# Performance work log

Measured on AMD Instinct MI355X. Metric: run time of the kernel, lower is better.

The kernel has to match this reference:

```python
import jax, jax.numpy as jnp
import numpy as np

N = 50000; C = 128; H0 = 256; H1 = 128; EM = 1000000; ES = 200000
INTENSITY = 10.0


def _ln(x, g, b):
    mu = jnp.mean(x, -1, keepdims=True)
    var = jnp.mean((x - mu) ** 2, -1, keepdims=True)
    return (x - mu) / jnp.sqrt(var + 1e-5) * g + b


def _sp_w(w):
    # PositiveLinear: softplus(raw_weight) + epsilon
    return jax.nn.softplus(w) + 1e-6


def _monotone(x, w0, b0, w1, b1, w2, b2):
    # MonotoneMap dims [1,32,32,1], Softplus activations between layers
    h = jax.nn.softplus(x @ _sp_w(w0).T + b0)
    h = jax.nn.softplus(h @ _sp_w(w1).T + b1)
    return h @ _sp_w(w2).T + b2


def _forward(nodes_latent, nbrs_latent, message_edgestr,
             W0, b0, g0, be0, W1, b1, g1, be1,
             Wp, bp, Ww, bw, sim_scale, sim_shift, coeff_raw,
             mm_w0, mm_b0, mm_w1, mm_b1, mm_w2, mm_b2,
             sup_src, sup_dst, msg_src, msg_dst):
    Nn = nodes_latent.shape[0]
    Es = sup_src.shape[0]
    M = 2 * Es
    # ---- congruence_score ----
    sup_query = jnp.concatenate([sup_src, sup_dst])      # [M]
    sup_partner = jnp.concatenate([sup_dst, sup_src])    # [M]
    partner_index = jnp.full((Nn,), -1, jnp.int32).at[sup_partner].max(jnp.arange(M, dtype=jnp.int32))
    pidx = partner_index[msg_dst]
    valid = pidx >= 0                                    # isin(msg_dst, sup_partner)
    # per masked message edge, query node = sup_query[partner_index[msg_dst]]; invalid -> dump segment Nn
    q = jnp.where(valid, sup_query[jnp.clip(pidx, 0)], Nn)
    qg = jnp.where(valid, q, 0)                          # safe gather index
    unit = nodes_latent / jnp.maximum(jnp.linalg.norm(nodes_latent, axis=-1, keepdims=True), 1e-8)
    cos = jnp.sum(unit[qg] * unit[msg_src], -1)          # cosine_similarity, [EM]
    scores = INTENSITY * cos
    segmax = jax.ops.segment_max(scores, q, num_segments=Nn + 1)
    e = jnp.exp(scores - jax.lax.stop_gradient(segmax)[q])
    denom = jax.ops.segment_sum(e, q, num_segments=Nn + 1)
    weights = e / denom[q]                               # scatter_softmax over query node
    cnt = jnp.maximum(jax.ops.segment_sum(jnp.ones_like(cos), q, num_segments=Nn + 1)[:Nn], 1.0)
    cong_node = jax.ops.segment_sum(weights * cos, q, num_segments=Nn + 1)[:Nn] / cnt  # scatter_mean
    exist = cong_node[sup_src] + cong_node[sup_dst]      # [Es]
    mm = _monotone(cos[:, None], mm_w0, mm_b0, mm_w1, mm_b1, mm_w2, mm_b2)[:, 0]
    weighted_edges = mm * message_edgestr
    strength_node = jax.ops.segment_sum(weighted_edges, q, num_segments=Nn + 1)[:Nn] / cnt
    strength = strength_node[sup_src] + strength_node[sup_dst]  # computed, discarded by original forward
    del strength
    # ---- main forward ----
    a = nodes_latent[sup_src] + nodes_latent[sup_dst]
    m = nodes_latent[sup_src] * nodes_latent[sup_dst]
    combined = jnp.concatenate([a, m], -1)               # [Es, 2C]
    h = jax.nn.relu(_ln(combined @ W0 + b0, g0, be0))
    ef = jax.nn.relu(_ln(h @ W1 + b1, g1, be1))          # edge_features [Es, H1]
    nbrs_sim = jnp.sum(nbrs_latent[sup_src] * nbrs_latent[sup_dst], -1, keepdims=True)
    P_cong = sim_scale * (exist[:, None] + sim_shift)
    P_nbr = sim_scale * (nbrs_sim + sim_shift)
    P_dec = ef @ Wp + bp
    u_c = jax.nn.softplus(coeff_raw)
    coeff = u_c / u_c.sum()                              # SoftplusSimplex
    logits = coeff * jnp.concatenate([P_dec, P_nbr, P_cong], -1)
    strengths = jax.nn.relu(jnp.concatenate([ef, nbrs_sim], -1) @ Ww + bw)
    return logits, strengths, coeff


def setup_inputs() -> dict:
    key = jax.random.key(0)
    ks = jax.random.split(key, 16)
    d = {}
    d['nodes_latent'] = jax.random.normal(ks[0], (N, C), jnp.float32)
    d['nbrs_latent'] = jax.random.normal(ks[1], (N, C), jnp.float32)
    d['sup_src'] = jax.random.randint(ks[2], (ES,), 0, N)
    d['sup_dst'] = jax.random.randint(ks[3], (ES,), 0, N)
    d['msg_src'] = jax.random.randint(ks[4], (EM,), 0, N)
    d['msg_dst'] = jax.random.randint(ks[5], (EM,), 0, N)
    d['message_edgestr'] = jax.random.uniform(ks[6], (EM,), jnp.float32)
    def lin(k, fi, fo):
        s = 1.0 / np.sqrt(fi)
        k1, k2 = jax.random.split(k)
        return (jax.random.uniform(k1, (fi, fo), jnp.float32, -s, s),
                jax.random.uniform(k2, (fo,), jnp.float32, -s, s))
    d['W0'], d['b0'] = lin(ks[7], 2 * C, H0)
    d['g0'] = jnp.ones((H0,), jnp.float32); d['be0'] = jnp.zeros((H0,), jnp.float32)
    d['W1'], d['b1'] = lin(ks[8], H0, H1)
    d['g1'] = jnp.ones((H1,), jnp.float32); d['be1'] = jnp.zeros((H1,), jnp.float32)
    d['Wp'], d['bp'] = lin(ks[9], H1, 1)
    d['Ww'], d['bw'] = lin(ks[10], H1 + 1, 1)
    d['sim_scale'] = jnp.float32(1.0)
    d['sim_shift'] = jnp.float32(0.0)
    d['coeff_raw'] = jnp.full((3,), 1.0 / 3.0, jnp.float32)
    d['mm_w0'] = jax.random.normal(ks[11], (32, 1), jnp.float32) * 0.01
    d['mm_b0'] = jnp.zeros((32,), jnp.float32)
    d['mm_w1'] = jax.random.normal(ks[12], (32, 32), jnp.float32) * 0.01
    d['mm_b1'] = jnp.zeros((32,), jnp.float32)
    d['mm_w2'] = jax.random.normal(ks[13], (1, 32), jnp.float32) * 0.01
    d['mm_b2'] = jnp.zeros((1,), jnp.float32)
    return d


def reference(nodes_latent, nbrs_latent, sup_src, sup_dst, msg_src, msg_dst, message_edgestr,
              W0, b0, g0, be0, W1, b1, g1, be1, Wp, bp, Ww, bw,
              sim_scale, sim_shift, coeff_raw,
              mm_w0, mm_b0, mm_w1, mm_b1, mm_w2, mm_b2):
    return _forward(nodes_latent, nbrs_latent, message_edgestr,
                    W0, b0, g0, be0, W1, b1, g1, be1,
                    Wp, bp, Ww, bw, sim_scale, sim_shift, coeff_raw,
                    mm_w0, mm_b0, mm_w1, mm_b1, mm_w2, mm_b2,
                    sup_src, sup_dst, msg_src, msg_dst)
```

## Files before the change

### kernel.cpp

```cpp
#include <hip/hip_runtime.h>
#include <math.h>

namespace {

constexpr int NN  = 50000;
constexpr int CC  = 128;
constexpr int EMn = 1000000;
constexpr int ESn = 200000;
constexpr int MLPB = 256;
constexpr int WPB  = 12;
constexpr int NTILES = ESn / 16;
constexpr int NWAVES = MLPB * WPB;

using i32x4 = __attribute__((ext_vector_type(4))) int;

__device__ __forceinline__ float softplusf(float x) {
  return (x > 20.f) ? x : log1pf(expf(x));
}
__device__ __forceinline__ int sdot4i(unsigned a, unsigned b, int c) {
#if __has_builtin(__builtin_amdgcn_sdot4)
  return __builtin_amdgcn_sdot4((int)a, (int)b, c, false);
#else
  int r = c;
#pragma unroll
  for (int k = 0; k < 4; k++) {
    int xa = ((int)(a << (24 - 8 * k))) >> 24;
    int xb = ((int)(b << (24 - 8 * k))) >> 24;
    r += xa * xb;
  }
  return r;
#endif
}
__device__ __forceinline__ unsigned pack4(float a, float b, float c, float d) {
  int ia = __float2int_rn(a), ib = __float2int_rn(b);
  int ic = __float2int_rn(c), id = __float2int_rn(d);
  return (unsigned)(ia & 255) | ((unsigned)(ib & 255) << 8) |
         ((unsigned)(ic & 255) << 16) | ((unsigned)(id & 255) << 24);
}

__global__ void k_init(int* __restrict__ pidx, double* __restrict__ dencnt,
                       float* __restrict__ num) {
  int i = blockIdx.x * blockDim.x + threadIdx.x;
  if (i < NN) { pidx[i] = -1; dencnt[i] = 0.0; num[i] = 0.f; }
}

__global__ void k_cvtq(const float* __restrict__ nodes, const float* __restrict__ nbrs,
                       char* __restrict__ qnodes, char* __restrict__ qunit,
                       char* __restrict__ qnbrs, float* __restrict__ nscale,
                       float* __restrict__ nbscale) {
  int row = blockIdx.x * 16 + (threadIdx.x >> 4);
  int li = threadIdx.x & 15;
  if (row >= 2 * NN) return;
  bool isn = row < NN;
  int r = isn ? row : row - NN;
  const float* src = (isn ? nodes : nbrs) + (size_t)r * CC;
  float4 x0 = *(const float4*)(src + li * 8);
  float4 x1 = *(const float4*)(src + li * 8 + 4);
  float v[8] = {x0.x, x0.y, x0.z, x0.w, x1.x, x1.y, x1.z, x1.w};
  float amax = 0.f, sq = 0.f;
#pragma unroll
  for (int j = 0; j < 8; j++) { amax = fmaxf(amax, fabsf(v[j])); sq += v[j] * v[j]; }
#pragma unroll
  for (int off = 1; off < 16; off <<= 1) {
    amax = fmaxf(amax, __shfl_xor(amax, off, 64));
    sq += __shfl_xor(sq, off, 64);
  }
  amax = fmaxf(amax, 1e-8f);
  float rs = 127.f / amax;
  uint2 p;
  p.x = pack4(v[0] * rs, v[1] * rs, v[2] * rs, v[3] * rs);
  p.y = pack4(v[4] * rs, v[5] * rs, v[6] * rs, v[7] * rs);
  if (isn) {
    *(uint2*)(qnodes + (size_t)r * CC + li * 8) = p;
    float ru = 127.f / fmaxf(sqrtf(sq), 1e-8f);
    uint2 pu;
    pu.x = pack4(v[0] * ru, v[1] * ru, v[2] * ru, v[3] * ru);
    pu.y = pack4(v[4] * ru, v[5] * ru, v[6] * ru, v[7] * ru);
    *(uint2*)(qunit + (size_t)r * CC + li * 8) = pu;
    if (li == 0) nscale[r] = amax / 127.f;
  } else {
    *(uint2*)(qnbrs + (size_t)r * CC + li * 8) = p;
    if (li == 0) nbscale[r] = amax / 127.f;
  }
}

__global__ void k_partner(const int* __restrict__ ss, const int* __restrict__ sd,
                          int* __restrict__ pidx) {
  int i = blockIdx.x * blockDim.x + threadIdx.x;
  if (i >= 2 * ESn) return;
  int partner = (i < ESn) ? sd[i] : ss[i - ESn];
  atomicMax(&pidx[partner], i);
}

__global__ void k_qnode(const int* __restrict__ pidx, const int* __restrict__ ss,
                        const int* __restrict__ sd, int* __restrict__ qnode) {
  int n = blockIdx.x * blockDim.x + threadIdx.x;
  if (n >= NN) return;
  int pi = pidx[n];
  qnode[n] = (pi < 0) ? -1 : ((pi < ESn) ? ss[pi] : sd[pi - ESn]);
}

__global__ __launch_bounds__(256) void k_prep2(const float* __restrict__ W0,
                                               const float* __restrict__ W1,
                                               char* __restrict__ w0q, char* __restrict__ w1q,
                                               float* __restrict__ cs0, float* __restrict__ cs1) {
  __shared__ float wmax[4];
  int c = blockIdx.x;
  int k = threadIdx.x;
  bool is0 = c < 256;
  int col = is0 ? c : c - 256;
  float v = is0 ? W0[(size_t)k * 256 + col] : W1[(size_t)k * 128 + col];
  float am = fabsf(v);
#pragma unroll
  for (int off = 1; off < 64; off <<= 1) am = fmaxf(am, __shfl_xor(am, off, 64));
  if ((k & 63) == 0) wmax[k >> 6] = am;
  __syncthreads();
  float amax = fmaxf(fmaxf(wmax[0], wmax[1]), fmaxf(wmax[2], wmax[3]));
  amax = fmaxf(amax, 1e-12f);
  int q = __float2int_rn(v * (127.f / amax));
  char* dst = is0 ? w0q : w1q;
  dst[(size_t)col * 256 + ((((k >> 4) ^ (col & 15))) << 4) + (k & 15)] = (char)q;
  if (k == 0) (is0 ? cs0 : cs1)[col] = amax / 127.f;
}

__global__ void k_cong(const double* __restrict__ dencnt, const float* __restrict__ num,
                       float* __restrict__ cong) {
  int n = blockIdx.x * blockDim.x + threadIdx.x;
  if (n >= NN) return;
  double dc = dencnt[n];
  double cnt = floor(dc * (1.0 / 4294967296.0) + 0.5);
  double den = dc - cnt * 4294967296.0;
  cong[n] = (cnt > 0.0) ? (float)(((double)num[n] / fmax(den, 1e-30)) / cnt) : 0.f;
}

__global__ void k_finish(const int* __restrict__ ssrc, const int* __restrict__ sdst,
                         const float* __restrict__ cong, const float* __restrict__ sscale,
                         const float* __restrict__ sshift, const float* __restrict__ craw,
                         float* __restrict__ out) {
  int i = blockIdx.x * blockDim.x + threadIdx.x;
  float u0 = softplusf(craw[0]), u1 = softplusf(craw[1]), u2 = softplusf(craw[2]);
  float usum = u0 + u1 + u2;
  float c2 = u2 / usum;
  if (i < ESn)
    out[3 * i + 2] = c2 * (sscale[0] * (cong[ssrc[i]] + cong[sdst[i]] + sshift[0]));
  if (i == 0) {
    out[4 * ESn + 0] = u0 / usum;
    out[4 * ESn + 1] = u1 / usum;
    out[4 * ESn + 2] = c2;
  }
}

__global__ __launch_bounds__(768, 3) void k_big(
    const char* __restrict__ qnodes, const float* __restrict__ nscale,
    const char* __restrict__ qnbrs, const float* __restrict__ nbscale,
    const char* __restrict__ qunit, const int* __restrict__ qnode,
    const int* __restrict__ ssrc, const int* __restrict__ sdst,
    const int* __restrict__ ms, const int* __restrict__ md,
    double* __restrict__ dencnt, float* __restrict__ num,
    const char* __restrict__ w0q, const char* __restrict__ w1q,
    const float* __restrict__ cs0g, const float* __restrict__ cs1g,
    const float* __restrict__ b0, const float* __restrict__ g0, const float* __restrict__ be0,
    const float* __restrict__ b1, const float* __restrict__ g1, const float* __restrict__ be1,
    const float* __restrict__ Wp, const float* __restrict__ bp,
    const float* __restrict__ Ww, const float* __restrict__ bw,
    const float* __restrict__ sscale, const float* __restrict__ sshift,
    const float* __restrict__ craw, float* __restrict__ out) {
  __shared__ char  w0s[65536];
  __shared__ char  w1s[32768];
  __shared__ float prm[1792];
  __shared__ char  hln[WPB][4096];

  const int t = threadIdx.x;
  for (int i = t; i < 4096; i += 768) ((uint4*)w0s)[i] = ((const uint4*)w0q)[i];
  for (int i = t; i < 2048; i += 768) ((uint4*)w1s)[i] = ((const uint4*)w1q)[i];
  if (t < 256) { prm[t] = cs0g[t]; prm[256 + t] = b0[t]; prm[512 + t] = g0[t]; prm[768 + t] = be0[t]; }
  if (t < 128) { prm[1024 + t] = cs1g[t]; prm[1152 + t] = b1[t]; prm[1280 + t] = g1[t];
                 prm[1408 + t] = be1[t];  prm[1536 + t] = Wp[t]; prm[1664 + t] = Ww[t]; }
  __syncthreads();

  const int wv = t >> 6, l = t & 63;
  const int e16 = l & 15, ch = l >> 4;
  const int gw = blockIdx.x * WPB + wv;
  char* hw = hln[wv];

  float u0 = softplusf(craw[0]), u1 = softplusf(craw[1]), u2 = softplusf(craw[2]);
  float us = u0 + u1 + u2, c0 = u0 / us, c1 = u1 / us;
  float sc = sscale[0], sh = sshift[0], bp0 = bp[0], bw0 = bw[0], ww128 = Ww[128];

  for (int tile = gw; tile < NTILES; tile += NWAVES) {
    const int s0 = tile * 16;
    int eg = s0 + e16;
    int es = ssrc[eg], ed = sdst[eg];
    float sxs = nscale[es], sxd = nscale[ed];
    const uint4* xp = (const uint4*)(qnodes + (size_t)es * CC);
    const uint4* yp = (const uint4*)(qnodes + (size_t)ed * CC);
    uint4 X0 = xp[ch], X1 = xp[4 + ch], Y0 = yp[ch], Y1 = yp[4 + ch];
    const uint4* nxp = (const uint4*)(qnbrs + (size_t)es * CC);
    const uint4* nyp = (const uint4*)(qnbrs + (size_t)ed * CC);
    uint4 NX0 = nxp[2 * ch], NX1 = nxp[2 * ch + 1];
    uint4 NY0 = nyp[2 * ch], NY1 = nyp[2 * ch + 1];
    float nbs = nbscale[es] * nbscale[ed];

    int sa = 0;
    sa = sdot4i(NX0.x, NY0.x, sa); sa = sdot4i(NX0.y, NY0.y, sa);
    sa = sdot4i(NX0.z, NY0.z, sa); sa = sdot4i(NX0.w, NY0.w, sa);
    sa = sdot4i(NX1.x, NY1.x, sa); sa = sdot4i(NX1.y, NY1.y, sa);
    sa = sdot4i(NX1.z, NY1.z, sa); sa = sdot4i(NX1.w, NY1.w, sa);
    sa += __shfl_xor(sa, 16, 64); sa += __shfl_xor(sa, 32, 64);
    float nsim = (float)sa * nbs;

    unsigned xw[8] = {X0.x, X0.y, X0.z, X0.w, X1.x, X1.y, X1.z, X1.w};
    unsigned yw[8] = {Y0.x, Y0.y, Y0.z, Y0.w, Y1.x, Y1.y, Y1.z, Y1.w};

    float amax = 1e-8f;
#pragma unroll
    for (int d = 0; d < 8; d++)
#pragma unroll
      for (int b = 0; b < 4; b++) {
        float fx = (float)((int)(xw[d] << (24 - 8 * b)) >> 24) * sxs;
        float fy = (float)((int)(yw[d] << (24 - 8 * b)) >> 24) * sxd;
        amax = fmaxf(amax, fmaxf(fabsf(fx + fy), fabsf(fx * fy)));
      }
    amax = fmaxf(amax, __shfl_xor(amax, 16, 64));
    amax = fmaxf(amax, __shfl_xor(amax, 32, 64));
    float rqz = 127.f / amax, rsc = amax / 127.f;

    i32x4 fr[4];
#pragma unroll
    for (int half = 0; half < 2; half++) {
#pragma unroll
      for (int d = 0; d < 4; d++) {
        unsigned xd = xw[half * 4 + d], yd = yw[half * 4 + d];
        float a_[4], m_[4];
#pragma unroll
        for (int b = 0; b < 4; b++) {
          float fx = (float)((int)(xd << (24 - 8 * b)) >> 24) * sxs;
          float fy = (float)((int)(yd << (24 - 8 * b)) >> 24) * sxd;
          a_[b] = fx + fy; m_[b] = fx * fy;
        }
        fr[half][d]     = (int)pack4(a_[0] * rqz, a_[1] * rqz, a_[2] * rqz, a_[3] * rqz);
        fr[2 + half][d] = (int)pack4(m_[0] * rqz, m_[1] * rqz, m_[2] * rqz, m_[3] * rqz);
      }
    }
    float rsrow[4];
#pragma unroll
    for (int j = 0; j < 4; j++) rsrow[j] = __shfl(rsc, (ch << 2) + j, 64);

    i32x4 acc[16];
#pragma unroll
    for (int nf = 0; nf < 16; nf++) acc[nf] = (i32x4){0, 0, 0, 0};
#pragma unroll
    for (int s = 0; s < 4; s++) {
      int gofs = (((s * 4 + ch) ^ e16) << 4);
#pragma unroll
      for (int nf = 0; nf < 16; nf++) {
        i32x4 bfr = *(const i32x4*)&w0s[(nf * 16 + e16) * 256 + gofs];
        acc[nf] = __builtin_amdgcn_mfma_i32_16x16x64_i8(fr[s], bfr, acc[nf], 0, 0, 0);
      }
    }

    float sj[4] = {0, 0, 0, 0}, qj[4] = {0, 0, 0, 0};
#pragma unroll
    for (int nf = 0; nf < 16; nf++) {
      float cs = prm[nf * 16 + e16], bb = prm[256 + nf * 16 + e16];
#pragma unroll
      for (int j = 0; j < 4; j++) {
        float h = (float)acc[nf][j] * rsrow[j] * cs + bb;
        sj[j] += h; qj[j] += h * h;
      }
    }
    float mu[4], rstd[4];
#pragma unroll
    for (int j = 0; j < 4; j++) {
      float s = sj[j], q = qj[j];
#pragma unroll
      for (int off = 1; off < 16; off <<= 1) { s += __shfl_xor(s, off, 64); q += __shfl_xor(q, off, 64); }
      mu[j] = s * (1.f / 256.f);
      rstd[j] = rsqrtf(q * (1.f / 256.f) - mu[j] * mu[j] + 1e-5f);
    }
    float hmax[4] = {1e-8f, 1e-8f, 1e-8f, 1e-8f};
#pragma unroll
    for (int nf = 0; nf < 16; nf++) {
      float cs = prm[nf * 16 + e16], bb = prm[256 + nf * 16 + e16];
      float gg = prm[512 + nf * 16 + e16], be = prm[768 + nf * 16 + e16];
#pragma unroll
      for (int j = 0; j < 4; j++) {
        float h = (float)acc[nf][j] * rsrow[j] * cs + bb;
        float v = fmaxf((h - mu[j]) * rstd[j] * gg + be, 0.f);
        hmax[j] = fmaxf(hmax[j], v);
        acc[nf][j] = __float_as_int(v);
      }
    }
    float rq2[4], rs2[4];
#pragma unroll
    for (int j = 0; j < 4; j++) {
      float m = hmax[j];
#pragma unroll
      for (int off = 1; off < 16; off <<= 1) m = fmaxf(m, __shfl_xor(m, off, 64));
      rq2[j] = 127.f / m; rs2[j] = m / 127.f;
    }
#pragma unroll
    for (int nf = 0; nf < 16; nf++) {
#pragma unroll
      for (int j = 0; j < 4; j++) {
        int r = (ch << 2) + j;
        int qv = __float2int_rn(__int_as_float(acc[nf][j]) * rq2[j]);
        hw[r * 256 + ((nf ^ r) << 4) + e16] = (char)qv;
      }
    }

    i32x4 acc2[8];
#pragma unroll
    for (int nf = 0; nf < 8; nf++) acc2[nf] = (i32x4){0, 0, 0, 0};
#pragma unroll
    for (int s = 0; s < 4; s++) {
      int gofs = (((s * 4 + ch) ^ e16) << 4);
      i32x4 af = *(const i32x4*)&hw[e16 * 256 + gofs];
#pragma unroll
      for (int nf = 0; nf < 8; nf++) {
        i32x4 bfr = *(const i32x4*)&w1s[(nf * 16 + e16) * 256 + gofs];
        acc2[nf] = __builtin_amdgcn_mfma_i32_16x16x64_i8(af, bfr, acc2[nf], 0, 0, 0);
      }
    }

    float s2[4] = {0, 0, 0, 0}, q2[4] = {0, 0, 0, 0};
#pragma unroll
    for (int nf = 0; nf < 8; nf++) {
      float cs = prm[1024 + nf * 16 + e16], bb = prm[1152 + nf * 16 + e16];
#pragma unroll
      for (int j = 0; j < 4; j++) {
        float ef = (float)acc2[nf][j] * rs2[j] * cs + bb;
        s2[j] += ef; q2[j] += ef * ef;
      }
    }
    float mu2[4], rstd2[4];
#pragma unroll
    for (int j = 0; j < 4; j++) {
      float s = s2[j], q = q2[j];
#pragma unroll
      for (int off = 1; off < 16; off <<= 1) { s += __shfl_xor(s, off, 64); q += __shfl_xor(q, off, 64); }
      mu2[j] = s * (1.f / 128.f);
      rstd2[j] = rsqrtf(q * (1.f / 128.f) - mu2[j] * mu2[j] + 1e-5f);
    }
    float pd[4] = {0, 0, 0, 0}, ws_[4] = {0, 0, 0, 0};
#pragma unroll
    for (int nf = 0; nf < 8; nf++) {
      float cs = prm[1024 + nf * 16 + e16], bb = prm[1152 + nf * 16 + e16];
      float gg = prm[1280 + nf * 16 + e16], be = prm[1408 + nf * 16 + e16];
      float wp_ = prm[1536 + nf * 16 + e16], ww_ = prm[1664 + nf * 16 + e16];
#pragma unroll
      for (int j = 0; j < 4; j++) {
        float ef = (float)acc2[nf][j] * rs2[j] * cs + bb;
        float v = fmaxf((ef - mu2[j]) * rstd2[j] * gg + be, 0.f);
        pd[j] += v * wp_; ws_[j] += v * ww_;
      }
    }
#pragma unroll
    for (int j = 0; j < 4; j++)
#pragma unroll
      for (int off = 1; off < 16; off <<= 1) {
        pd[j] += __shfl_xor(pd[j], off, 64);
        ws_[j] += __shfl_xor(ws_[j], off, 64);
      }
    float nsr[4];
#pragma unroll
    for (int j = 0; j < 4; j++) nsr[j] = __shfl(nsim, (ch << 2) + j, 64);
    if (e16 == 0) {
#pragma unroll
      for (int j = 0; j < 4; j++) {
        int sidx = s0 + (ch << 2) + j;
        out[3 * sidx + 0] = c0 * (pd[j] + bp0);
        out[3 * sidx + 1] = c1 * (sc * (nsr[j] + sh));
        out[3 * ESn + sidx] = fmaxf(ws_[j] + nsr[j] * ww128 + bw0, 0.f);
      }
    }
  }

  const int li8 = l & 7, grp = l >> 3;
  for (int i = gw; i < EMn / 8; i += NWAVES) {
    int e = i * 8 + grp;
    int q = qnode[md[e]];
    if (q < 0) continue;
    int s = ms[e];
    uint4 a = ((const uint4*)(qunit + (size_t)q * CC))[li8];
    uint4 b = ((const uint4*)(qunit + (size_t)s * CC))[li8];
    int acc = 0;
    acc = sdot4i(a.x, b.x, acc); acc = sdot4i(a.y, b.y, acc);
    acc = sdot4i(a.z, b.z, acc); acc = sdot4i(a.w, b.w, acc);
    acc += __shfl_xor(acc, 1, 64);
    acc += __shfl_xor(acc, 2, 64);
    acc += __shfl_xor(acc, 4, 64);
    if (li8 == 0) {
      float cv = (float)acc * (1.0f / (127.f * 127.f));
      float wvv = expf(10.0f * cv);
      atomicAdd(&dencnt[q], (double)wvv + 4294967296.0);
      atomicAdd(&num[q], wvv * cv);
    }
  }
}

}

extern "C" void kernel_launch(void* const* d_in, const int* in_sizes, int n_in,
                              void* d_out, int out_size, void* d_ws, size_t ws_size,
                              hipStream_t stream) {
  (void)in_sizes; (void)n_in; (void)out_size; (void)ws_size;
  const float* nodes  = (const float*)d_in[0];
  const float* nbrs   = (const float*)d_in[1];
  const int* sup_src  = (const int*)d_in[2];
  const int* sup_dst  = (const int*)d_in[3];
  const int* msg_src  = (const int*)d_in[4];
  const int* msg_dst  = (const int*)d_in[5];
  const float* W0  = (const float*)d_in[7];
  const float* b0  = (const float*)d_in[8];
  const float* g0  = (const float*)d_in[9];
  const float* be0 = (const float*)d_in[10];
  const float* W1  = (const float*)d_in[11];
  const float* b1  = (const float*)d_in[12];
  const float* g1  = (const float*)d_in[13];
  const float* be1 = (const float*)d_in[14];
  const float* Wp  = (const float*)d_in[15];
  const float* bp  = (const float*)d_in[16];
  const float* Ww  = (const float*)d_in[17];
  const float* bw  = (const float*)d_in[18];
  const float* sscale = (const float*)d_in[19];
  const float* sshift = (const float*)d_in[20];
  const float* craw   = (const float*)d_in[21];
  float* out = (float*)d_out;

  char* p = (char*)d_ws;
  auto take = [&](size_t bytes) -> char* {
    char* r = p; p += (bytes + 255) & ~(size_t)255; return r;
  };
  char*   w0q     = take((size_t)256 * 256);
  char*   w1q     = take((size_t)128 * 256);
  float*  cs0     = (float*)take((size_t)256 * 4);
  float*  cs1     = (float*)take((size_t)128 * 4);
  char*   qnodes  = take((size_t)NN * CC);
  char*   qunit   = take((size_t)NN * CC);
  char*   qnbrs   = take((size_t)NN * CC);
  float*  nscale  = (float*)take((size_t)NN * 4);
  float*  nbscale = (float*)take((size_t)NN * 4);
  int*    pidx    = (int*)take((size_t)NN * 4);
  int*    qnode   = (int*)take((size_t)NN * 4);
  double* dencnt  = (double*)take((size_t)NN * 8);
  float*  num     = (float*)take((size_t)NN * 4);
  float*  cong    = (float*)take((size_t)NN * 4);

  k_init<<<(NN + 255) / 256, 256, 0, stream>>>(pidx, dencnt, num);
  k_cvtq<<<(2 * NN + 15) / 16, 256, 0, stream>>>(nodes, nbrs, qnodes, qunit, qnbrs,
                                                 nscale, nbscale);
  k_prep2<<<384, 256, 0, stream>>>(W0, W1, w0q, w1q, cs0, cs1);
  k_partner<<<(2 * ESn + 255) / 256, 256, 0, stream>>>(sup_src, sup_dst, pidx);
  k_qnode<<<(NN + 255) / 256, 256, 0, stream>>>(pidx, sup_src, sup_dst, qnode);
  k_big<<<MLPB, 768, 0, stream>>>(qnodes, nscale, qnbrs, nbscale, qunit, qnode,
                                  sup_src, sup_dst, msg_src, msg_dst, dencnt, num,
                                  w0q, w1q, cs0, cs1, b0, g0, be0, b1, g1, be1,
                                  Wp, bp, Ww, bw, sscale, sshift, craw, out);
  k_cong<<<(NN + 255) / 256, 256, 0, stream>>>(dencnt, num, cong);
  k_finish<<<(ESn + 255) / 256, 256, 0, stream>>>(sup_src, sup_dst, cong,
                                                  sscale, sshift, craw, out);
}
```

Before: 244.9 us.

## Prefetch next MLP tile gathers and restructure message-edge cosine loop

The support-edge MLP loop now issues the gathers for the next tile before computing the current one, so global-load latency overlaps the int8 matrix work. A separate pass precomputes each message edge's query node, with invalid edges sent to a zeroed dump row and dump accumulator slot. This removes the data-dependent skip and double indirection from the cosine loop, which now uses 4 lanes per edge with 16 edges per wave and exp2f. Launch bounds are relaxed to one block per SM to leave registers for the prefetch. The cost is an extra kernel, a 4 MB index array, and atomic work spent on invalid edges that land in the dump slot.

```diff
diff --git a/kernel.cpp b/kernel.cpp
--- a/kernel.cpp
+++ b/kernel.cpp
@@ -39,9 +39,11 @@
 }
 
 __global__ void k_init(int* __restrict__ pidx, double* __restrict__ dencnt,
-                       float* __restrict__ num) {
+                       float* __restrict__ num, char* __restrict__ qunit) {
   int i = blockIdx.x * blockDim.x + threadIdx.x;
-  if (i < NN) { pidx[i] = -1; dencnt[i] = 0.0; num[i] = 0.f; }
+  if (i < NN) pidx[i] = -1;
+  if (i <= NN) { dencnt[i] = 0.0; num[i] = 0.f; }
+  if (i < CC / 4) ((unsigned*)(qunit + (size_t)NN * CC))[i] = 0u;
 }
 
 __global__ void k_cvtq(const float* __restrict__ nodes, const float* __restrict__ nbrs,
@@ -100,6 +102,14 @@
   qnode[n] = (pi < 0) ? -1 : ((pi < ESn) ? ss[pi] : sd[pi - ESn]);
 }
 
+__global__ void k_qedge(const int* __restrict__ md, const int* __restrict__ qnode,
+                        int* __restrict__ qedge) {
+  int e = blockIdx.x * blockDim.x + threadIdx.x;
+  if (e >= EMn) return;
+  int q = qnode[md[e]];
+  qedge[e] = (q < 0) ? NN : q;
+}
+
 __global__ __launch_bounds__(256) void k_prep2(const float* __restrict__ W0,
                                                const float* __restrict__ W1,
                                                char* __restrict__ w0q, char* __restrict__ w1q,
@@ -150,12 +160,12 @@
   }
 }
 
-__global__ __launch_bounds__(768, 3) void k_big(
+__global__ __launch_bounds__(768, 1) void k_big(
     const char* __restrict__ qnodes, const float* __restrict__ nscale,
     const char* __restrict__ qnbrs, const float* __restrict__ nbscale,
-    const char* __restrict__ qunit, const int* __restrict__ qnode,
+    const char* __restrict__ qunit, const int* __restrict__ qedge,
     const int* __restrict__ ssrc, const int* __restrict__ sdst,
-    const int* __restrict__ ms, const int* __restrict__ md,
+    const int* __restrict__ ms,
     double* __restrict__ dencnt, float* __restrict__ num,
     const char* __restrict__ w0q, const char* __restrict__ w1q,
     const float* __restrict__ cs0g, const float* __restrict__ cs1g,
@@ -187,19 +197,24 @@
   float us = u0 + u1 + u2, c0 = u0 / us, c1 = u1 / us;
   float sc = sscale[0], sh = sshift[0], bp0 = bp[0], bw0 = bw[0], ww128 = Ww[128];
 
-  for (int tile = gw; tile < NTILES; tile += NWAVES) {
-    const int s0 = tile * 16;
-    int eg = s0 + e16;
+  int tile = gw;
+  float sxs = 0.f, sxd = 0.f, nbs = 0.f;
+  uint4 X0 = {}, X1 = {}, Y0 = {}, Y1 = {}, NX0 = {}, NX1 = {}, NY0 = {}, NY1 = {};
+  if (tile < NTILES) {
+    int eg = tile * 16 + e16;
     int es = ssrc[eg], ed = sdst[eg];
-    float sxs = nscale[es], sxd = nscale[ed];
+    sxs = nscale[es]; sxd = nscale[ed];
+    nbs = nbscale[es] * nbscale[ed];
     const uint4* xp = (const uint4*)(qnodes + (size_t)es * CC);
     const uint4* yp = (const uint4*)(qnodes + (size_t)ed * CC);
-    uint4 X0 = xp[ch], X1 = xp[4 + ch], Y0 = yp[ch], Y1 = yp[4 + ch];
+    X0 = xp[ch]; X1 = xp[4 + ch]; Y0 = yp[ch]; Y1 = yp[4 + ch];
     const uint4* nxp = (const uint4*)(qnbrs + (size_t)es * CC);
     const uint4* nyp = (const uint4*)(qnbrs + (size_t)ed * CC);
-    uint4 NX0 = nxp[2 * ch], NX1 = nxp[2 * ch + 1];
-    uint4 NY0 = nyp[2 * ch], NY1 = nyp[2 * ch + 1];
-    float nbs = nbscale[es] * nbscale[ed];
+    NX0 = nxp[2 * ch]; NX1 = nxp[2 * ch + 1]; NY0 = nyp[2 * ch]; NY1 = nyp[2 * ch + 1];
+  }
+
+  while (tile < NTILES) {
+    const int s0 = tile * 16;
 
     int sa = 0;
     sa = sdot4i(NX0.x, NY0.x, sa); sa = sdot4i(NX0.y, NY0.y, sa);
@@ -246,6 +261,20 @@
 #pragma unroll
     for (int j = 0; j < 4; j++) rsrow[j] = __shfl(rsc, (ch << 2) + j, 64);
 
+    const int ntile = tile + NWAVES;
+    if (ntile < NTILES) {
+      int eg = ntile * 16 + e16;
+      int es = ssrc[eg], ed = sdst[eg];
+      sxs = nscale[es]; sxd = nscale[ed];
+      nbs = nbscale[es] * nbscale[ed];
+      const uint4* xp = (const uint4*)(qnodes + (size_t)es * CC);
+      const uint4* yp = (const uint4*)(qnodes + (size_t)ed * CC);
+      X0 = xp[ch]; X1 = xp[4 + ch]; Y0 = yp[ch]; Y1 = yp[4 + ch];
+      const uint4* nxp = (const uint4*)(qnbrs + (size_t)es * CC);
+      const uint4* nyp = (const uint4*)(qnbrs + (size_t)ed * CC);
+      NX0 = nxp[2 * ch]; NX1 = nxp[2 * ch + 1]; NY0 = nyp[2 * ch]; NY1 = nyp[2 * ch + 1];
+    }
+
     i32x4 acc[16];
 #pragma unroll
     for (int nf = 0; nf < 16; nf++) acc[nf] = (i32x4){0, 0, 0, 0};
@@ -374,25 +403,29 @@
         out[3 * ESn + sidx] = fmaxf(ws_[j] + nsr[j] * ww128 + bw0, 0.f);
       }
     }
-  }
-
-  const int li8 = l & 7, grp = l >> 3;
-  for (int i = gw; i < EMn / 8; i += NWAVES) {
-    int e = i * 8 + grp;
-    int q = qnode[md[e]];
-    if (q < 0) continue;
+    tile = ntile;
+  }
+
+  const int li4 = l & 3, grp4 = l >> 2;
+#pragma unroll 2
+  for (int i = gw; i < EMn / 16; i += NWAVES) {
+    int e = i * 16 + grp4;
+    int q = qedge[e];
     int s = ms[e];
-    uint4 a = ((const uint4*)(qunit + (size_t)q * CC))[li8];
-    uint4 b = ((const uint4*)(qunit + (size_t)s * CC))[li8];
+    const uint4* ap = (const uint4*)(qunit + (size_t)q * CC);
+    const uint4* bp2 = (const uint4*)(qunit + (size_t)s * CC);
+    uint4 a0 = ap[li4], a1 = ap[4 + li4];
+    uint4 b0_ = bp2[li4], b1_ = bp2[4 + li4];
     int acc = 0;
-    acc = sdot4i(a.x, b.x, acc); acc = sdot4i(a.y, b.y, acc);
-    acc = sdot4i(a.z, b.z, acc); acc = sdot4i(a.w, b.w, acc);
+    acc = sdot4i(a0.x, b0_.x, acc); acc = sdot4i(a0.y, b0_.y, acc);
+    acc = sdot4i(a0.z, b0_.z, acc); acc = sdot4i(a0.w, b0_.w, acc);
+    acc = sdot4i(a1.x, b1_.x, acc); acc = sdot4i(a1.y, b1_.y, acc);
+    acc = sdot4i(a1.z, b1_.z, acc); acc = sdot4i(a1.w, b1_.w, acc);
     acc += __shfl_xor(acc, 1, 64);
     acc += __shfl_xor(acc, 2, 64);
-    acc += __shfl_xor(acc, 4, 64);
-    if (li8 == 0) {
+    if (li4 == 0) {
       float cv = (float)acc * (1.0f / (127.f * 127.f));
-      float wvv = expf(10.0f * cv);
+      float wvv = exp2f(cv * 14.4269504089f);
       atomicAdd(&dencnt[q], (double)wvv + 4294967296.0);
       atomicAdd(&num[q], wvv * cv);
     }
@@ -437,24 +470,26 @@
   float*  cs0     = (float*)take((size_t)256 * 4);
   float*  cs1     = (float*)take((size_t)128 * 4);
   char*   qnodes  = take((size_t)NN * CC);
-  char*   qunit   = take((size_t)NN * CC);
+  char*   qunit   = take((size_t)(NN + 1) * CC);
   char*   qnbrs   = take((size_t)NN * CC);
   float*  nscale  = (float*)take((size_t)NN * 4);
   float*  nbscale = (float*)take((size_t)NN * 4);
   int*    pidx    = (int*)take((size_t)NN * 4);
   int*    qnode   = (int*)take((size_t)NN * 4);
-  double* dencnt  = (double*)take((size_t)NN * 8);
-  float*  num     = (float*)take((size_t)NN * 4);
+  int*    qedge   = (int*)take((size_t)EMn * 4);
+  double* dencnt  = (double*)take((size_t)(NN + 1) * 8);
+  float*  num     = (float*)take((size_t)(NN + 1) * 4);
   float*  cong    = (float*)take((size_t)NN * 4);
 
-  k_init<<<(NN + 255) / 256, 256, 0, stream>>>(pidx, dencnt, num);
+  k_init<<<(NN + 1 + 255) / 256, 256, 0, stream>>>(pidx, dencnt, num, qunit);
   k_cvtq<<<(2 * NN + 15) / 16, 256, 0, stream>>>(nodes, nbrs, qnodes, qunit, qnbrs,
                                                  nscale, nbscale);
   k_prep2<<<384, 256, 0, stream>>>(W0, W1, w0q, w1q, cs0, cs1);
   k_partner<<<(2 * ESn + 255) / 256, 256, 0, stream>>>(sup_src, sup_dst, pidx);
   k_qnode<<<(NN + 255) / 256, 256, 0, stream>>>(pidx, sup_src, sup_dst, qnode);
-  k_big<<<MLPB, 768, 0, stream>>>(qnodes, nscale, qnbrs, nbscale, qunit, qnode,
-                                  sup_src, sup_dst, msg_src, msg_dst, dencnt, num,
+  k_qedge<<<(EMn + 255) / 256, 256, 0, stream>>>(msg_dst, qnode, qedge);
+  k_big<<<MLPB, 768, 0, stream>>>(qnodes, nscale, qnbrs, nbscale, qunit, qedge,
+                                  sup_src, sup_dst, msg_src, dencnt, num,
                                   w0q, w1q, cs0, cs1, b0, g0, be0, b1, g1, be1,
                                   Wp, bp, Ww, bw, sscale, sshift, craw, out);
   k_cong<<<(NN + 255) / 256, 256, 0, stream>>>(dencnt, num, cong);
```

Result: no change. 246.4 us (+0.6%).
